# Performance work log

Measured on AMD Instinct MI355X. Metric: run time of the kernel, lower is better.

The kernel has to match this reference:

```python
import jax, jax.numpy as jnp
import numpy as np

N = 50000      # num nodes
E = 800000     # num edges (avg degree 16)
IN_FEA = 256
OU_FEA = 64


def setup_inputs() -> dict:
    key = jax.random.key(0)
    k_h, k_w, k_r, k_c, k_v = jax.random.split(key, 5)
    h = jax.random.normal(k_h, (N, IN_FEA), dtype=jnp.float32)
    # Linear(in_fea, ou_fea, bias=None): weight applied as h @ W, W [IN, OUT]
    W = jax.random.normal(k_w, (IN_FEA, OU_FEA), dtype=jnp.float32) / np.sqrt(IN_FEA)
    row = jax.random.randint(k_r, (E,), 0, N, dtype=jnp.int32)
    col = jax.random.randint(k_c, (E,), 0, N, dtype=jnp.int32)
    vals = jax.random.uniform(k_v, (E,), dtype=jnp.float32)
    return {"h": h, "W": W, "row": row, "col": col, "vals": vals}


def reference(h, W, row, col, vals):
    # dense projection: [N, IN] @ [IN, OUT] -> [N, OUT]
    hp = h @ W
    # torch builds sparse tensor with indices [col, row], i.e. G = A^T,
    # so torch.sparse.mm(G, hp)[i] = sum over edges with col==i of vals * hp[row]
    msg = hp[row] * vals[:, None]                      # [E, OUT] gather + scale
    out = jax.ops.segment_sum(msg, col, num_segments=N)  # scatter-add to dest
    return out
```

## Files before the change

### kernel.cpp

```cpp
#include <hip/hip_runtime.h>
#include <hip/hip_bf16.h>

#define IN_F 256
#define OU_F 64
#define BKN 128
#define BSHIFT 7
#define NBMAX 512
#define PCHUNK 2048
#define STAGE_CAP 4096
#define NHIST 64

typedef __attribute__((ext_vector_type(8))) short short8;
typedef __attribute__((ext_vector_type(4))) float f32x4;

__device__ inline short8 cvt8(float4 a, float4 b)
{
    union { short8 s8; __hip_bfloat162 h2[4]; } u;
    u.h2[0] = __float22bfloat162_rn(make_float2(a.x, a.y));
    u.h2[1] = __float22bfloat162_rn(make_float2(a.z, a.w));
    u.h2[2] = __float22bfloat162_rn(make_float2(b.x, b.y));
    u.h2[3] = __float22bfloat162_rn(make_float2(b.z, b.w));
    return u.s8;
}

__global__ void __launch_bounds__(512, 4)
fused_gemm_hist(const float* __restrict__ h, const float* __restrict__ W,
                __hip_bfloat16* __restrict__ hp, const int* __restrict__ col,
                int* __restrict__ bcnt, int* __restrict__ boffs,
                int* __restrict__ bcursor, int N, int E, int NB)
{
    union Sh {
        unsigned short Wt[64][264];
        struct { int lh[NBMAX]; int s[256]; } hh;
    };
    __shared__ Sh sh;
    __shared__ int isLast;
    const int t   = threadIdx.x;
    const int bid = blockIdx.x;

    if (bid < NHIST) {
        for (int i = t; i < NBMAX; i += 512) sh.hh.lh[i] = 0;
        __syncthreads();
        const int n4 = E >> 2;
        const int4* c4 = (const int4*)col;
        for (int i = bid * 512 + t; i < n4; i += NHIST * 512) {
            int4 v = c4[i];
            atomicAdd(&sh.hh.lh[v.x >> BSHIFT], 1);
            atomicAdd(&sh.hh.lh[v.y >> BSHIFT], 1);
            atomicAdd(&sh.hh.lh[v.z >> BSHIFT], 1);
            atomicAdd(&sh.hh.lh[v.w >> BSHIFT], 1);
        }
        if (bid == 0)
            for (int e = (n4 << 2) + t; e < E; e += 512)
                atomicAdd(&sh.hh.lh[col[e] >> BSHIFT], 1);
        __syncthreads();
        for (int i = t; i < NB; i += 512)
            if (sh.hh.lh[i]) atomicAdd(&bcnt[i], sh.hh.lh[i]);
        __threadfence();
        __syncthreads();
        if (t == 0) {
            int v = atomicAdd(&bcnt[NBMAX], 1);
            isLast = (v == NHIST - 1);
        }
        __syncthreads();
        if (!isLast) return;

        for (int i = t; i < NB; i += 512)
            sh.hh.lh[i] = __hip_atomic_load(&bcnt[i], __ATOMIC_RELAXED,
                                            __HIP_MEMORY_SCOPE_AGENT);
        __syncthreads();
        int s0 = 0, s1 = 0;
        if (t < 256) {
            s0 = sh.hh.lh[2 * t];
            s1 = s0 + sh.hh.lh[2 * t + 1];
            sh.hh.s[t] = s1;
        }
        __syncthreads();
        for (int d = 1; d < 256; d <<= 1) {
            int v = (t < 256 && t >= d) ? sh.hh.s[t - d] : 0;
            __syncthreads();
            if (t < 256) sh.hh.s[t] += v;
            __syncthreads();
        }
        if (t < 256) {
            int excl = t ? sh.hh.s[t - 1] : 0;
            int i0 = 2 * t, i1 = 2 * t + 1;
            if (i0 < NB) { boffs[i0] = excl;      bcursor[i0] = excl;      }
            if (i1 < NB) { boffs[i1] = excl + s0; bcursor[i1] = excl + s0; }
            if (t == 255) boffs[NB] = sh.hh.s[255];
        }
        return;
    }

    const int tb = bid - NHIST;
#pragma unroll
    for (int i = 0; i < 16; ++i) {
        int p  = t + i * 512;
        int c  = p & 63;
        int k0 = (p >> 6) << 1;
        float x = W[(size_t)k0 * OU_F + c];
        float y = W[(size_t)(k0 + 1) * OU_F + c];
        __hip_bfloat162 bb = __float22bfloat162_rn(make_float2(x, y));
        *reinterpret_cast<unsigned*>(&sh.Wt[c][k0]) = *reinterpret_cast<unsigned*>(&bb);
    }
    __syncthreads();

    const int l   = t & 63;
    const int wv  = t >> 6;
    const int cl  = l & 15;
    const int kg  = l >> 4;
    const int rg4 = wv & 3;
    const int cg  = wv >> 2;

    short8 bfr[2][8];
#pragma unroll
    for (int nt2 = 0; nt2 < 2; ++nt2)
#pragma unroll
        for (int ks = 0; ks < 8; ++ks)
            bfr[nt2][ks] = *reinterpret_cast<const short8*>(
                &sh.Wt[cg * 32 + nt2 * 16 + cl][ks * 32 + kg * 8]);

#pragma unroll
    for (int tt = 0; tt < 2; ++tt) {
        const int rbase = tb * 128 + tt * 64 + rg4 * 16;
        const int r     = rbase + cl;
        const int rld   = min(r, N - 1);
        const float4* hrow = reinterpret_cast<const float4*>(h) + (size_t)rld * (IN_F / 4);

        f32x4 acc0 = (f32x4){0.f, 0.f, 0.f, 0.f};
        f32x4 acc1 = (f32x4){0.f, 0.f, 0.f, 0.f};
#pragma unroll
        for (int ks = 0; ks < 8; ++ks) {
            float4 a0 = hrow[ks * 8 + kg * 2];
            float4 a1 = hrow[ks * 8 + kg * 2 + 1];
            short8 af = cvt8(a0, a1);
            acc0 = __builtin_amdgcn_mfma_f32_16x16x32_bf16(af, bfr[0][ks], acc0, 0, 0, 0);
            acc1 = __builtin_amdgcn_mfma_f32_16x16x32_bf16(af, bfr[1][ks], acc1, 0, 0, 0);
        }
#pragma unroll
        for (int rg = 0; rg < 4; ++rg) {
            int rr = rbase + kg * 4 + rg;
            if (rr < N) {
                size_t base = (size_t)rr * OU_F + cg * 32 + cl;
                hp[base]      = __float2bfloat16(acc0[rg]);
                hp[base + 16] = __float2bfloat16(acc1[rg]);
            }
        }
    }
}

__global__ void __launch_bounds__(512, 4)
partition_kernel(const int* __restrict__ row, const int* __restrict__ col,
                 const float* __restrict__ vals, int* __restrict__ bcursor,
                 int2* __restrict__ epk, int E, int NB)
{
    __shared__ int  hist[NBMAX];
    __shared__ int  X[NBMAX];
    __shared__ int  gshift[NBMAX];
    __shared__ int  s[256];
    __shared__ int2 stage[PCHUNK];

    const int t = threadIdx.x;
    const int base = blockIdx.x * PCHUNK;
    const int n = min(PCHUNK, E - base);

    for (int i = t; i < NBMAX; i += 512) hist[i] = 0;
    __syncthreads();

#pragma unroll
    for (int k = 0; k < PCHUNK / 512; ++k) {
        int i = t + k * 512;
        if (i < n) atomicAdd(&hist[col[base + i] >> BSHIFT], 1);
    }
    __syncthreads();

    int h0 = 0, h1 = 0;
    if (t < 256) {
        h0 = hist[2 * t];
        h1 = h0 + hist[2 * t + 1];
        s[t] = h1;
    }
    __syncthreads();
    for (int d = 1; d < 256; d <<= 1) {
        int v = (t < 256 && t >= d) ? s[t - d] : 0;
        __syncthreads();
        if (t < 256) s[t] += v;
        __syncthreads();
    }
    if (t < 256) {
        int excl = t ? s[t - 1] : 0;
        X[2 * t]     = excl;
        X[2 * t + 1] = excl + h0;
    }
    __syncthreads();

    for (int i = t; i < NB; i += 512) {
        int hc = hist[i];
        int g = hc ? atomicAdd(&bcursor[i], hc) : 0;
        gshift[i] = g - X[i];
    }
    __syncthreads();

#pragma unroll
    for (int k = 0; k < PCHUNK / 512; ++k) {
        int i = t + k * 512;
        if (i < n) {
            int e  = base + i;
            int cv = col[e];
            int b  = cv >> BSHIFT;
            int r  = atomicAdd(&X[b], 1);
            unsigned pk = (unsigned)row[e] | ((unsigned)(cv & (BKN - 1)) << 17);
            stage[r] = make_int2((int)pk, __float_as_int(vals[e]));
        }
    }
    __syncthreads();

    const int l = t & 63, wv = t >> 6;
    for (int b = wv; b < NB; b += 8) {
        int cnt = hist[b];
        if (!cnt) continue;
        int src0 = X[b] - cnt;
        int dst0 = gshift[b] + src0;
        for (int j = l; j < cnt; j += 64)
            epk[dst0 + j] = stage[src0 + j];
    }
}

__global__ void __launch_bounds__(512)
csr_kernel(const int2* __restrict__ epk, const int* __restrict__ boffs,
           int2* __restrict__ epk2, int* __restrict__ node_offs,
           int N, int NB)
{
    __shared__ int  cnt[BKN];
    __shared__ int  cur[BKN];
    __shared__ int2 stage[STAGE_CAP];
    const int t = threadIdx.x;
    const int b = blockIdx.x;
    const int s = boffs[b], e = boffs[b + 1];
    const int n = e - s;
    const int node0 = b << BSHIFT;

    if (t < BKN) cnt[t] = 0;
    __syncthreads();
    for (int i = t; i < n; i += 512)
        atomicAdd(&cnt[((unsigned)epk[s + i].x) >> 17], 1);
    __syncthreads();

    if (t < 64) {
        int v0 = cnt[2 * t], v1 = cnt[2 * t + 1];
        int p = v0 + v1, sum = p;
#pragma unroll
        for (int d = 1; d < 64; d <<= 1) {
            int u = __shfl_up(sum, d);
            if (t >= d) sum += u;
        }
        int excl = sum - p;
        cur[2 * t]     = excl;
        cur[2 * t + 1] = excl + v0;
        int nd0 = node0 + 2 * t;
        if (nd0 < N)     node_offs[nd0]     = s + excl;
        if (nd0 + 1 < N) node_offs[nd0 + 1] = s + excl + v0;
    }
    if (b == NB - 1 && t == 0) node_offs[N] = e;
    __syncthreads();

    if (n <= STAGE_CAP) {
        for (int i = t; i < n; i += 512) {
            int2 r = epk[s + i];
            int pos = atomicAdd(&cur[((unsigned)r.x) >> 17], 1);
            stage[pos] = r;
        }
        __syncthreads();
        for (int i = t; i < n; i += 512)
            epk2[s + i] = stage[i];
    } else {
        for (int i = t; i < n; i += 512) {
            int2 r = epk[s + i];
            int pos = atomicAdd(&cur[((unsigned)r.x) >> 17], 1);
            epk2[s + pos] = r;
        }
    }
}

__global__ void __launch_bounds__(256)
gather_kernel(const __hip_bfloat16* __restrict__ hp, const int* __restrict__ node_offs,
              const int2* __restrict__ epk2, float* __restrict__ out, int N)
{
    int wid  = (int)((blockIdx.x * 256u + threadIdx.x) >> 6);
    int lane = threadIdx.x & 63;
    if (wid >= N) return;
    int s = node_offs[wid], e = node_offs[wid + 1];
    float acc = 0.f;
    for (int base = s; base < e; base += 64) {
        int n = min(64, e - base);
        int2 m = make_int2(0, 0);
        if (lane < n) m = epk2[base + lane];
        int j = 0;
        for (; j + 4 <= n; j += 4) {
            unsigned r0 = (unsigned)__shfl(m.x, j)     & 0x1FFFFu;
            unsigned r1 = (unsigned)__shfl(m.x, j + 1) & 0x1FFFFu;
            unsigned r2 = (unsigned)__shfl(m.x, j + 2) & 0x1FFFFu;
            unsigned r3 = (unsigned)__shfl(m.x, j + 3) & 0x1FFFFu;
            float v0 = __int_as_float(__shfl(m.y, j));
            float v1 = __int_as_float(__shfl(m.y, j + 1));
            float v2 = __int_as_float(__shfl(m.y, j + 2));
            float v3 = __int_as_float(__shfl(m.y, j + 3));
            float x0 = __bfloat162float(hp[((size_t)r0 << 6) + lane]);
            float x1 = __bfloat162float(hp[((size_t)r1 << 6) + lane]);
            float x2 = __bfloat162float(hp[((size_t)r2 << 6) + lane]);
            float x3 = __bfloat162float(hp[((size_t)r3 << 6) + lane]);
            acc = fmaf(v0, x0, acc);
            acc = fmaf(v1, x1, acc);
            acc = fmaf(v2, x2, acc);
            acc = fmaf(v3, x3, acc);
        }
        for (; j < n; ++j) {
            unsigned r = (unsigned)__shfl(m.x, j) & 0x1FFFFu;
            float    v = __int_as_float(__shfl(m.y, j));
            acc = fmaf(v, __bfloat162float(hp[((size_t)r << 6) + lane]), acc);
        }
    }
    out[(size_t)wid * OU_F + lane] = acc;
}

__global__ void __launch_bounds__(256)
scatter_kernel(const __hip_bfloat16* __restrict__ hp, const int* __restrict__ row,
               const int* __restrict__ col, const float* __restrict__ vals,
               float* __restrict__ out, int E)
{
    unsigned int gid = blockIdx.x * 256u + threadIdx.x;
    int e = (int)(gid >> 6);
    if (e >= E) return;
    int f = (int)(gid & 63u);
    int r = row[e], c = col[e];
    float m = vals[e] * __bfloat162float(hp[(size_t)r * OU_F + f]);
    __hip_atomic_fetch_add(&out[(size_t)c * OU_F + f], m,
                           __ATOMIC_RELAXED, __HIP_MEMORY_SCOPE_AGENT);
}

extern "C" void kernel_launch(void* const* d_in, const int* in_sizes, int n_in,
                              void* d_out, int out_size, void* d_ws, size_t ws_size,
                              hipStream_t stream)
{
    const float* h    = (const float*)d_in[0];
    const float* W    = (const float*)d_in[1];
    const int*   row  = (const int*)d_in[2];
    const int*   col  = (const int*)d_in[3];
    const float* vals = (const float*)d_in[4];
    float*       out  = (float*)d_out;

    const int N = in_sizes[0] / IN_F;
    const int E = in_sizes[2];
    const int NB = (N + BKN - 1) / BKN;

    char*  ws  = (char*)d_ws;
    size_t off = 0;
    auto alloc = [&](size_t bytes) -> char* {
        char* p = ws + off;
        off = (off + bytes + 255) & ~(size_t)255;
        return p;
    };
    __hip_bfloat16* hp = (__hip_bfloat16*)alloc((size_t)N * OU_F * 2);
    int*   bcnt      = (int*)  alloc((size_t)(NBMAX + 1) * 4);
    int*   boffs     = (int*)  alloc((size_t)(NBMAX + 1) * 4);
    int*   bcursor   = (int*)  alloc((size_t)NBMAX * 4);
    int*   node_offs = (int*)  alloc((size_t)(N + 1) * 4);
    int2*  epk       = (int2*) alloc((size_t)E * 8);
    int2*  epk2      = (int2*) alloc((size_t)E * 8);
    const bool fits = (off <= ws_size) && (NB <= NBMAX) && (N < 131072);

    const int ntiles2 = (N + 127) / 128;

    if (fits) {
        hipMemsetAsync(bcnt, 0, (size_t)(NBMAX + 1) * 4, stream);
        fused_gemm_hist<<<NHIST + ntiles2, 512, 0, stream>>>(
            h, W, hp, col, bcnt, boffs, bcursor, N, E, NB);
        partition_kernel<<<(E + PCHUNK - 1) / PCHUNK, 512, 0, stream>>>(
            row, col, vals, bcursor, epk, E, NB);
        csr_kernel<<<NB, 512, 0, stream>>>(epk, boffs, epk2, node_offs, N, NB);
        gather_kernel<<<(N + 3) / 4, 256, 0, stream>>>(hp, node_offs, epk2, out, N);
    } else {
        hipMemsetAsync(bcnt, 0, (size_t)(NBMAX + 1) * 4, stream);
        fused_gemm_hist<<<NHIST + ntiles2, 512, 0, stream>>>(
            h, W, hp, col, bcnt, boffs, bcursor, N, E, NB);
        hipMemsetAsync(d_out, 0, (size_t)out_size * sizeof(float), stream);
        unsigned long long total = (unsigned long long)E * 64ull;
        unsigned int sgrid = (unsigned int)((total + 255ull) / 256ull);
        scatter_kernel<<<sgrid, 256, 0, stream>>>(hp, row, col, vals, out, E);
    }
}
```

Measured before the change: 105.3 us.

## Reorder gemm/hist blocks, enlarge partition chunks, flatten scatter write-out

The GEMM tiles are moved to the low block indices so they are scheduled first, and the histogram blocks are raised from 64 to 256 and placed at the end. The partition chunk size doubles to 4096 edges, and each edge's global destination is now stored in shared memory. The final write-out becomes a flat per-element scatter instead of a per-bucket loop over warps. This targets launch ordering, poor load balance in the per-bucket copy, and the count of global cursor atomics. In exchange it uses more shared memory per partition block and makes global writes less contiguous. It also adds a bounds guard on the histogram scan.

```diff
diff --git a/kernel.cpp b/kernel.cpp
--- a/kernel.cpp
+++ b/kernel.cpp
@@ -6,9 +6,9 @@
 #define BKN 128
 #define BSHIFT 7
 #define NBMAX 512
-#define PCHUNK 2048
+#define CHUNK 4096
 #define STAGE_CAP 4096
-#define NHIST 64
+#define NHIST 256
 
 typedef __attribute__((ext_vector_type(8))) short short8;
 typedef __attribute__((ext_vector_type(4))) float f32x4;
@@ -27,7 +27,7 @@
 fused_gemm_hist(const float* __restrict__ h, const float* __restrict__ W,
                 __hip_bfloat16* __restrict__ hp, const int* __restrict__ col,
                 int* __restrict__ bcnt, int* __restrict__ boffs,
-                int* __restrict__ bcursor, int N, int E, int NB)
+                int* __restrict__ bcursor, int N, int E, int NB, int ntiles2)
 {
     union Sh {
         unsigned short Wt[64][264];
@@ -38,19 +38,20 @@
     const int t   = threadIdx.x;
     const int bid = blockIdx.x;
 
-    if (bid < NHIST) {
+    if (bid >= ntiles2) {
+        const int hb = bid - ntiles2;
         for (int i = t; i < NBMAX; i += 512) sh.hh.lh[i] = 0;
         __syncthreads();
         const int n4 = E >> 2;
         const int4* c4 = (const int4*)col;
-        for (int i = bid * 512 + t; i < n4; i += NHIST * 512) {
+        for (int i = hb * 512 + t; i < n4; i += NHIST * 512) {
             int4 v = c4[i];
             atomicAdd(&sh.hh.lh[v.x >> BSHIFT], 1);
             atomicAdd(&sh.hh.lh[v.y >> BSHIFT], 1);
             atomicAdd(&sh.hh.lh[v.z >> BSHIFT], 1);
             atomicAdd(&sh.hh.lh[v.w >> BSHIFT], 1);
         }
-        if (bid == 0)
+        if (hb == 0)
             for (int e = (n4 << 2) + t; e < E; e += 512)
                 atomicAdd(&sh.hh.lh[col[e] >> BSHIFT], 1);
         __syncthreads();
@@ -71,8 +72,9 @@
         __syncthreads();
         int s0 = 0, s1 = 0;
         if (t < 256) {
-            s0 = sh.hh.lh[2 * t];
-            s1 = s0 + sh.hh.lh[2 * t + 1];
+            int i0 = 2 * t, i1 = 2 * t + 1;
+            s0 = (i0 < NB) ? sh.hh.lh[i0] : 0;
+            s1 = s0 + ((i1 < NB) ? sh.hh.lh[i1] : 0);
             sh.hh.s[t] = s1;
         }
         __syncthreads();
@@ -92,7 +94,6 @@
         return;
     }
 
-    const int tb = bid - NHIST;
 #pragma unroll
     for (int i = 0; i < 16; ++i) {
         int p  = t + i * 512;
@@ -122,7 +123,7 @@
 
 #pragma unroll
     for (int tt = 0; tt < 2; ++tt) {
-        const int rbase = tb * 128 + tt * 64 + rg4 * 16;
+        const int rbase = bid * 128 + tt * 64 + rg4 * 16;
         const int r     = rbase + cl;
         const int rld   = min(r, N - 1);
         const float4* hrow = reinterpret_cast<const float4*>(h) + (size_t)rld * (IN_F / 4);
@@ -149,7 +150,7 @@
     }
 }
 
-__global__ void __launch_bounds__(512, 4)
+__global__ void __launch_bounds__(512)
 partition_kernel(const int* __restrict__ row, const int* __restrict__ col,
                  const float* __restrict__ vals, int* __restrict__ bcursor,
                  int2* __restrict__ epk, int E, int NB)
@@ -158,51 +159,53 @@
     __shared__ int  X[NBMAX];
     __shared__ int  gshift[NBMAX];
     __shared__ int  s[256];
-    __shared__ int2 stage[PCHUNK];
+    __shared__ int2 stage[CHUNK];
+    __shared__ int  gpos[CHUNK];
 
     const int t = threadIdx.x;
-    const int base = blockIdx.x * PCHUNK;
-    const int n = min(PCHUNK, E - base);
+    const int base = blockIdx.x * CHUNK;
+    const int n = min(CHUNK, E - base);
 
     for (int i = t; i < NBMAX; i += 512) hist[i] = 0;
     __syncthreads();
 
 #pragma unroll
-    for (int k = 0; k < PCHUNK / 512; ++k) {
+    for (int k = 0; k < CHUNK / 512; ++k) {
         int i = t + k * 512;
         if (i < n) atomicAdd(&hist[col[base + i] >> BSHIFT], 1);
     }
     __syncthreads();
 
-    int h0 = 0, h1 = 0;
+    int s0 = 0, s1 = 0;
     if (t < 256) {
-        h0 = hist[2 * t];
-        h1 = h0 + hist[2 * t + 1];
-        s[t] = h1;
+        int idx = t * 2;
+        s0 = hist[idx];
+        s1 = s0 + hist[idx + 1];
+        s[t] = s1;
     }
     __syncthreads();
     for (int d = 1; d < 256; d <<= 1) {
-        int v = (t < 256 && t >= d) ? s[t - d] : 0;
+        int v = (t >= d && t < 256) ? s[t - d] : 0;
         __syncthreads();
         if (t < 256) s[t] += v;
         __syncthreads();
     }
     if (t < 256) {
-        int excl = t ? s[t - 1] : 0;
-        X[2 * t]     = excl;
-        X[2 * t + 1] = excl + h0;
+        int excl = (t > 0) ? s[t - 1] : 0;
+        X[t * 2]     = excl;
+        X[t * 2 + 1] = excl + s0;
     }
     __syncthreads();
 
     for (int i = t; i < NB; i += 512) {
-        int hc = hist[i];
-        int g = hc ? atomicAdd(&bcursor[i], hc) : 0;
+        int hcnt = hist[i];
+        int g = hcnt ? atomicAdd(&bcursor[i], hcnt) : 0;
         gshift[i] = g - X[i];
     }
     __syncthreads();
 
 #pragma unroll
-    for (int k = 0; k < PCHUNK / 512; ++k) {
+    for (int k = 0; k < CHUNK / 512; ++k) {
         int i = t + k * 512;
         if (i < n) {
             int e  = base + i;
@@ -211,18 +214,15 @@
             int r  = atomicAdd(&X[b], 1);
             unsigned pk = (unsigned)row[e] | ((unsigned)(cv & (BKN - 1)) << 17);
             stage[r] = make_int2((int)pk, __float_as_int(vals[e]));
-        }
-    }
-    __syncthreads();
-
-    const int l = t & 63, wv = t >> 6;
-    for (int b = wv; b < NB; b += 8) {
-        int cnt = hist[b];
-        if (!cnt) continue;
-        int src0 = X[b] - cnt;
-        int dst0 = gshift[b] + src0;
-        for (int j = l; j < cnt; j += 64)
-            epk[dst0 + j] = stage[src0 + j];
+            gpos[r]  = gshift[b] + r;
+        }
+    }
+    __syncthreads();
+
+#pragma unroll
+    for (int k = 0; k < CHUNK / 512; ++k) {
+        int i = t + k * 512;
+        if (i < n) epk[gpos[i]] = stage[i];
     }
 }
 
@@ -371,18 +371,16 @@
 
     const int ntiles2 = (N + 127) / 128;
 
+    hipMemsetAsync(bcnt, 0, (size_t)(NBMAX + 1) * 4, stream);
+    fused_gemm_hist<<<ntiles2 + NHIST, 512, 0, stream>>>(
+        h, W, hp, col, bcnt, boffs, bcursor, N, E, NB, ntiles2);
+
     if (fits) {
-        hipMemsetAsync(bcnt, 0, (size_t)(NBMAX + 1) * 4, stream);
-        fused_gemm_hist<<<NHIST + ntiles2, 512, 0, stream>>>(
-            h, W, hp, col, bcnt, boffs, bcursor, N, E, NB);
-        partition_kernel<<<(E + PCHUNK - 1) / PCHUNK, 512, 0, stream>>>(
+        partition_kernel<<<(E + CHUNK - 1) / CHUNK, 512, 0, stream>>>(
             row, col, vals, bcursor, epk, E, NB);
         csr_kernel<<<NB, 512, 0, stream>>>(epk, boffs, epk2, node_offs, N, NB);
         gather_kernel<<<(N + 3) / 4, 256, 0, stream>>>(hp, node_offs, epk2, out, N);
     } else {
-        hipMemsetAsync(bcnt, 0, (size_t)(NBMAX + 1) * 4, stream);
-        fused_gemm_hist<<<NHIST + ntiles2, 512, 0, stream>>>(
-            h, W, hp, col, bcnt, boffs, bcursor, N, E, NB);
         hipMemsetAsync(d_out, 0, (size_t)out_size * sizeof(float), stream);
         unsigned long long total = (unsigned long long)E * 64ull;
         unsigned int sgrid = (unsigned int)((total + 255ull) / 256ull);
```

Result: slower. 145.9 us (+38.6%).
